# Kernel tuning notes

Hardware: AMD Instinct MI355X
Metric: run time of the kernel (lower is better)

## Reference

```python
import jax, jax.numpy as jnp
import numpy as np

# --- batched state-vector quantum circuit sim: AngleEmbedding(RY) + BasicEntanglerLayers(RX + ring CNOT) ---

def _ry(state, theta, wire, n):
    # per-sample RY(theta) on `wire`; state: (B,) + (2,)*n complex
    ax = wire + 1
    c = jnp.cos(0.5 * theta).reshape((-1,) + (1,) * (n - 1)).astype(state.dtype)
    s = jnp.sin(0.5 * theta).reshape((-1,) + (1,) * (n - 1)).astype(state.dtype)
    s0 = jnp.take(state, 0, axis=ax)
    s1 = jnp.take(state, 1, axis=ax)
    return jnp.stack([c * s0 - s * s1, s * s0 + c * s1], axis=ax)

def _rx(state, theta, wire, n):
    # scalar RX(theta) on `wire` (shared weight across batch)
    ax = wire + 1
    c = jnp.cos(0.5 * theta).astype(state.dtype)
    s = (-1j * jnp.sin(0.5 * theta)).astype(state.dtype)
    s0 = jnp.take(state, 0, axis=ax)
    s1 = jnp.take(state, 1, axis=ax)
    return jnp.stack([c * s0 + s * s1, s * s0 + c * s1], axis=ax)

def _cnot(state, ctrl, tgt):
    ax_c = ctrl + 1
    s0 = jnp.take(state, 0, axis=ax_c)
    s1 = jnp.take(state, 1, axis=ax_c)
    ax_t = tgt + 1 if tgt < ctrl else tgt  # target axis index after removing ctrl axis
    s1 = jnp.flip(s1, axis=ax_t)
    return jnp.stack([s0, s1], axis=ax_c)

def _circuit(x_qin, qweights):
    # x_qin: (Bn, n) angles; qweights: (L, n)
    Bn, n = x_qin.shape
    state = jnp.zeros((Bn,) + (2,) * n, jnp.complex64)
    state = state.at[(slice(None),) + (0,) * n].set(1.0)
    for w in range(n):  # AngleEmbedding, rotation='Y'
        state = _ry(state, x_qin[:, w], w, n)
    for l in range(qweights.shape[0]):  # BasicEntanglerLayers
        for w in range(n):
            state = _rx(state, qweights[l, w], w, n)
        for w in range(n):
            state = _cnot(state, w, (w + 1) % n)
    probs = jnp.real(state * jnp.conj(state))
    outs = []
    for w in range(n):  # <Z_w> = P(bit_w=0) - P(bit_w=1)
        axes = tuple(a for a in range(1, n + 1) if a != w + 1)
        p = probs.sum(axis=axes)  # (Bn, 2)
        outs.append(p[:, 0] - p[:, 1])
    return jnp.stack(outs, axis=-1).astype(jnp.float32)


def setup_inputs() -> dict:
    key = jax.random.key(0)
    ks = jax.random.split(key, 9)
    B, N, H, NQ, L = 16, 1024, 256, 8, 2
    x = jax.random.normal(ks[0], (B, N, H), jnp.float32)
    norm_adj = jax.random.uniform(ks[1], (N, N), jnp.float32) / N
    Wg = jax.random.normal(ks[2], (H, H), jnp.float32) * 0.02
    bg = jax.random.normal(ks[3], (H,), jnp.float32) * 0.02
    Wpre = jax.random.normal(ks[4], (NQ, H), jnp.float32) * 0.05
    bpre = jax.random.normal(ks[5], (NQ,), jnp.float32) * 0.02
    qweights = jax.random.uniform(ks[6], (L, NQ), jnp.float32) * (2.0 * np.pi)
    Wpost = jax.random.normal(ks[7], (H, NQ), jnp.float32) * 0.1
    bpost = jax.random.normal(ks[8], (H,), jnp.float32) * 0.02
    return {"x": x, "norm_adj": norm_adj, "Wg": Wg, "bg": bg, "Wpre": Wpre,
            "bpre": bpre, "qweights": qweights, "Wpost": Wpost, "bpost": bpost}


def reference(x, norm_adj, Wg, bg, Wpre, bpre, qweights, Wpost, bpost):
    # GCN aggregation + GELU(Linear)  (dropout is identity in eval mode)
    x_agg = jnp.einsum('ij,bjh->bih', norm_adj, x)
    x_agg = jax.nn.gelu(x_agg @ Wg.T + bg, approximate=False)
    B, N, H = x_agg.shape
    x_flat = x_agg.reshape(B * N, H).astype(jnp.float32)
    x_qin = jnp.tanh(x_flat @ Wpre.T + bpre) * np.pi
    q_out = _circuit(x_qin, qweights)          # (B*N, n_qubits)
    out = (q_out @ Wpost.T + bpost).reshape(B, N, H)
    return out
```

## Files before the change

### kernel.cpp

```cpp
#include <hip/hip_runtime.h>
#include <math.h>

typedef __attribute__((ext_vector_type(8))) short bf16x8;
typedef _Float16 f16x8 __attribute__((ext_vector_type(8)));
typedef __attribute__((ext_vector_type(4))) float f32x4;

#define PI_F 3.14159265358979323846f

__device__ __forceinline__ unsigned short f2bf(float f) {
  unsigned int u = __float_as_uint(f);
  u += 0x7FFFu + ((u >> 16) & 1u);
  return (unsigned short)(u >> 16);
}

__device__ __forceinline__ float bf2f(unsigned short u) {
  return __uint_as_float(((unsigned int)u) << 16);
}

__device__ __forceinline__ void async_ld16(const unsigned short* g, unsigned short* l) {
  __builtin_amdgcn_global_load_lds(
      (const __attribute__((address_space(1))) void*)g,
      (__attribute__((address_space(3))) void*)l,
      16, 0, 0);
}

__device__ __forceinline__ float fast_erf(float x) {
  float a = fabsf(x);
  float t = 1.0f / fmaf(0.3275911f, a, 1.0f);
  float p = t * fmaf(t, fmaf(t, fmaf(t, fmaf(t, 1.061405429f, -1.453152027f),
                                     1.421413741f), -0.284496736f), 0.254829592f);
  float e = __expf(-a * a);
  float r = 1.0f - p * e;
  return copysignf(r, x);
}

__device__ __forceinline__ float fast_tanh(float a) {
  float e = __expf(2.0f * a);
  return 1.0f - 2.0f / (e + 1.0f);
}

template<int ML, int MR>
__device__ __forceinline__ void apply_rx(float re[4], float im[4], float c, float s) {
  float pr[4], pi[4];
  #pragma unroll
  for (int r = 0; r < 4; r++) {
    float vr = re[r ^ MR], vi = im[r ^ MR];
    if (ML) { vr = __shfl_xor(vr, ML, 64); vi = __shfl_xor(vi, ML, 64); }
    pr[r] = vr; pi[r] = vi;
  }
  #pragma unroll
  for (int r = 0; r < 4; r++) {
    re[r] = fmaf(c, re[r],  s * pi[r]);
    im[r] = fmaf(c, im[r], -s * pr[r]);
  }
}

__global__ __launch_bounds__(256)
void prep_kernel(const float* __restrict__ adj, unsigned short* __restrict__ adj_bf,
                 const float* __restrict__ Wg, unsigned short* __restrict__ Wg_bf,
                 const float* __restrict__ qw, unsigned short* __restrict__ Uri,
                 const float* __restrict__ Wpost, _Float16* __restrict__ Gt,
                 const float* __restrict__ x, unsigned short* __restrict__ xT) {
  __shared__ float smem[1056];
  int bid = blockIdx.x, t = threadIdx.x;
  if (bid < 1024) {
    int i = bid * 256 + t;
    float4 v = ((const float4*)adj)[i];
    ushort4 o; o.x = f2bf(v.x); o.y = f2bf(v.y); o.z = f2bf(v.z); o.w = f2bf(v.w);
    ((ushort4*)adj_bf)[i] = o;
  } else if (bid < 1088) {
    int i = (bid - 1024) * 256 + t;
    float4 v = ((const float4*)Wg)[i];
    ushort4 o; o.x = f2bf(v.x); o.y = f2bf(v.y); o.z = f2bf(v.z); o.w = f2bf(v.w);
    ((ushort4*)Wg_bf)[i] = o;
  } else if (bid < 1152) {
    if (t < 16) { smem[t] = cosf(0.5f * qw[t]); smem[16 + t] = sinf(0.5f * qw[t]); }
    __syncthreads();
    int wv = t >> 6, L = t & 63;
    int k = (bid - 1088) * 4 + wv;
    float re[4], im[4];
    #pragma unroll
    for (int r = 0; r < 4; r++) { re[r] = (r * 64 + L == k) ? 1.f : 0.f; im[r] = 0.f; }
    apply_rx<1, 0>(re, im, smem[0], smem[16]);
    apply_rx<2, 0>(re, im, smem[1], smem[17]);
    apply_rx<4, 0>(re, im, smem[2], smem[18]);
    apply_rx<8, 0>(re, im, smem[3], smem[19]);
    apply_rx<16, 0>(re, im, smem[4], smem[20]);
    apply_rx<32, 0>(re, im, smem[5], smem[21]);
    apply_rx<0, 1>(re, im, smem[6], smem[22]);
    apply_rx<0, 2>(re, im, smem[7], smem[23]);
    apply_rx<3, 0>(re, im, smem[8], smem[24]);
    apply_rx<6, 0>(re, im, smem[9], smem[25]);
    apply_rx<12, 0>(re, im, smem[10], smem[26]);
    apply_rx<24, 0>(re, im, smem[11], smem[27]);
    apply_rx<48, 0>(re, im, smem[12], smem[28]);
    apply_rx<32, 1>(re, im, smem[13], smem[29]);
    apply_rx<0, 3>(re, im, smem[14], smem[30]);
    apply_rx<3, 2>(re, im, smem[15], smem[31]);
    const int M[8] = {0xAB, 0xFD, 0xFA, 0xF5, 0xEA, 0xD5, 0xAA, 0x55};
    #pragma unroll
    for (int r = 0; r < 4; r++) {
      int n = 0;
      #pragma unroll
      for (int w = 0; w < 8; w++) {
        int bit = (__popc(L & (M[w] & 63)) ^ __popc((r << 6) & M[w])) & 1;
        n |= bit << w;
      }
      int row_re = ((n >> 4) << 5) + (n & 15);
      Uri[(size_t)row_re * 256 + k] = f2bf(re[r]);
      Uri[(size_t)(row_re + 16) * 256 + k] = f2bf(im[r]);
    }
  } else if (bid < 1168) {
    int tid = (bid - 1152) * 256 + t;
    int h = tid >> 4;
    int n0 = (tid & 15) << 4;
    float wv8[8];
    #pragma unroll
    for (int w = 0; w < 8; w++) wv8[w] = Wpost[h * 8 + w];
    #pragma unroll
    for (int j = 0; j < 16; j++) {
      int n = n0 + j;
      float sum = 0.f;
      #pragma unroll
      for (int w = 0; w < 8; w++) sum += ((n >> w) & 1) ? -wv8[w] : wv8[w];
      Gt[h * 256 + n] = (_Float16)sum;
    }
  } else {
    int tb = bid - 1168;
    int jt = tb & 31, ht = (tb >> 5) & 7, bb = tb >> 8;
    int tx = t & 31, ty = t >> 5;
    const float* xb = x + (size_t)bb * 1024 * 256;
    #pragma unroll
    for (int i = 0; i < 4; i++) {
      int j = jt * 32 + ty + i * 8;
      smem[(ty + i * 8) * 33 + tx] = xb[(size_t)j * 256 + ht * 32 + tx];
    }
    __syncthreads();
    unsigned short* xTb = xT + (size_t)bb * 256 * 1024;
    #pragma unroll
    for (int i = 0; i < 4; i++) {
      int h = ht * 32 + ty + i * 8;
      xTb[(size_t)h * 1024 + jt * 32 + tx] = f2bf(smem[tx * 33 + ty + i * 8]);
    }
  }
}

__global__ __launch_bounds__(256)
void gemm1_kernel(const unsigned short* __restrict__ A,
                  const unsigned short* __restrict__ Bt,
                  unsigned short* __restrict__ C,
                  int K, int tilesN, int ldC) {
  __shared__ unsigned short As[2 * 64 * 32];
  __shared__ unsigned short Bs[2 * 128 * 32];
  int bid = blockIdx.x;
  int swz = (bid & 7) * 64 + (bid >> 3);
  int in_ = swz >> 4;
  int im  = swz & 15;
  const unsigned short* Ab  = A  + (long long)im * 64 * K;
  const unsigned short* Btb = Bt + (long long)in_ * 128 * K;

  int t = threadIdx.x;
  int wv = t >> 6, lane = t & 63;
  int wm = wv >> 1, wn = wv & 1;
  int l15 = lane & 15, quad = lane >> 4;

  f32x4 acc[2][4] = {};

  for (int kk = 0; kk < K; kk += 64) {
    __syncthreads();
    #pragma unroll
    for (int kb = 0; kb < 2; kb++) {
      {
        int r = t >> 2, c = (t & 3) ^ ((r >> 1) & 3);
        async_ld16(Ab + (long long)r * K + kk + kb * 32 + c * 8, &As[kb * 2048 + t * 8]);
      }
      #pragma unroll
      for (int q = 0; q < 2; q++) {
        int sidx = q * 256 + t;
        int r = sidx >> 2, c = (sidx & 3) ^ ((r >> 1) & 3);
        async_ld16(Btb + (long long)r * K + kk + kb * 32 + c * 8, &Bs[kb * 4096 + sidx * 8]);
      }
    }
    __syncthreads();
    #pragma unroll
    for (int kb = 0; kb < 2; kb++) {
      bf16x8 af[2], bfr[4];
      #pragma unroll
      for (int mt = 0; mt < 2; mt++) {
        int row = wm * 32 + mt * 16 + l15;
        af[mt] = *(const bf16x8*)&As[kb * 2048 + row * 32 + ((quad ^ ((row >> 1) & 3)) * 8)];
      }
      #pragma unroll
      for (int nt = 0; nt < 4; nt++) {
        int row = wn * 64 + nt * 16 + l15;
        bfr[nt] = *(const bf16x8*)&Bs[kb * 4096 + row * 32 + ((quad ^ ((row >> 1) & 3)) * 8)];
      }
      #pragma unroll
      for (int mt = 0; mt < 2; mt++)
        #pragma unroll
        for (int nt = 0; nt < 4; nt++)
          acc[mt][nt] = __builtin_amdgcn_mfma_f32_16x16x32_bf16(af[mt], bfr[nt], acc[mt][nt], 0, 0, 0);
    }
  }

  int n0 = in_ * 128;
  #pragma unroll
  for (int mt = 0; mt < 2; mt++) {
    #pragma unroll
    for (int nt = 0; nt < 4; nt++) {
      int colg = n0 + wn * 64 + nt * 16 + l15;
      #pragma unroll
      for (int r = 0; r < 4; r++) {
        int rowg = im * 64 + wm * 32 + mt * 16 + quad * 4 + r;
        C[(size_t)rowg * ldC + colg] = f2bf(acc[mt][nt][r]);
      }
    }
  }
}

__global__ __launch_bounds__(1024, 4)
void qfused_kernel(const unsigned short* __restrict__ xagg,
                   const unsigned short* __restrict__ Wg,
                   const float* __restrict__ bg,
                   const float* __restrict__ Wpre, const float* __restrict__ bpre,
                   const unsigned short* __restrict__ Uri,
                   const _Float16* __restrict__ Gt,
                   const float* __restrict__ bpost,
                   float* __restrict__ out) {
  __shared__ __align__(16) char smemraw[102400];
  unsigned short* As  = (unsigned short*)smemraw;
  unsigned short* gs  = (unsigned short*)(smemraw + 32768);
  _Float16*       Ts  = (_Float16*)(smemraw + 32768);
  unsigned short* P0s = (unsigned short*)(smemraw + 65536);
  float*          prt = (float*)(smemraw + 65536);
  float*          csw = (float*)(smemraw + 98304);

  int t = threadIdx.x;
  int wv = t >> 6, lane = t & 63;
  int l15 = lane & 15, quad = lane >> 4;

  const unsigned short* Ab = xagg + (size_t)blockIdx.x * 64 * 256;

  #pragma unroll
  for (int q = 0; q < 2; q++) {
    int sidx = q * 1024 + t;
    int kb = sidx >> 8;
    int r  = (sidx >> 2) & 63;
    int c  = (sidx & 3) ^ ((r >> 1) & 3);
    async_ld16(Ab + (size_t)r * 256 + kb * 32 + c * 8, &As[sidx * 8]);
  }
  __syncthreads();

  f32x4 acc[4] = {};
  {
    const unsigned short* Wp = Wg + (size_t)(wv * 16 + l15) * 256 + quad * 8;
    bf16x8 wf[2];
    wf[0] = *(const bf16x8*)(Wp);
    wf[1] = *(const bf16x8*)(Wp + 32);
    #pragma unroll
    for (int k8 = 0; k8 < 8; k8++) {
      int cur = k8 & 1;
      #pragma unroll
      for (int mt = 0; mt < 4; mt++) {
        int row = mt * 16 + l15;
        bf16x8 af = *(const bf16x8*)&As[k8 * 2048 + row * 32 + ((quad ^ ((row >> 1) & 3)) * 8)];
        acc[mt] = __builtin_amdgcn_mfma_f32_16x16x32_bf16(af, wf[cur], acc[mt], 0, 0, 0);
      }
      if (k8 < 6) wf[cur] = *(const bf16x8*)(Wp + (k8 + 2) * 32);
    }
  }
  {
    int col = wv * 16 + l15;
    float bgl = bg[col];
    int kbc = col >> 5, chunk = (col >> 3) & 3, e = col & 7;
    #pragma unroll
    for (int mt = 0; mt < 4; mt++) {
      #pragma unroll
      for (int r = 0; r < 4; r++) {
        int row = mt * 16 + quad * 4 + r;
        float v = acc[mt][r] + bgl;
        v = 0.5f * v * (1.0f + fast_erf(v * 0.7071067811865475f));
        *(unsigned short*)((char*)gs + kbc * 4096 + row * 64 +
                           ((chunk ^ ((row >> 1) & 3)) << 4) + e * 2) = f2bf(v);
      }
    }
  }
  __syncthreads();

  {
    int k8 = wv >> 1, mh = wv & 1;
    const float* wrow = Wpre + (size_t)(l15 & 7) * 256 + k8 * 32 + quad * 8;
    float4 wa = *(const float4*)wrow;
    float4 wb = *(const float4*)(wrow + 4);
    float v8[8] = {wa.x, wa.y, wa.z, wa.w, wb.x, wb.y, wb.z, wb.w};
    bf16x8 whi, wlo;
    #pragma unroll
    for (int j = 0; j < 8; j++) {
      unsigned short h = f2bf(v8[j]);
      whi[j] = (short)h;
      wlo[j] = (short)f2bf(v8[j] - bf2f(h));
    }
    f32x4 aacc[2] = {};
    #pragma unroll
    for (int mt = 0; mt < 2; mt++) {
      int row = mh * 32 + mt * 16 + l15;
      bf16x8 ga = *(const bf16x8*)((char*)gs + k8 * 4096 + row * 64 +
                                   ((quad ^ ((row >> 1) & 3)) << 4));
      aacc[mt] = __builtin_amdgcn_mfma_f32_16x16x32_bf16(ga, whi, aacc[mt], 0, 0, 0);
      aacc[mt] = __builtin_amdgcn_mfma_f32_16x16x32_bf16(ga, wlo, aacc[mt], 0, 0, 0);
    }
    if (l15 < 8) {
      #pragma unroll
      for (int mt = 0; mt < 2; mt++)
        #pragma unroll
        for (int r = 0; r < 4; r++)
          prt[k8 * 512 + (mh * 32 + mt * 16 + quad * 4 + r) * 8 + l15] = aacc[mt][r];
    }
  }
  __syncthreads();

  if (t < 512) {
    float s = 0.f;
    #pragma unroll
    for (int k = 0; k < 8; k++) s += prt[k * 512 + t];
    float th = (0.5f * PI_F) * fast_tanh(s + bpre[t & 7]);
    int row = t >> 3, w = t & 7;
    csw[row * 16 + w] = __cosf(th);
    csw[row * 16 + 8 + w] = __sinf(th);
  }
  __syncthreads();

  #pragma unroll
  for (int rr = 0; rr < 4; rr++) {
    int row = wv * 4 + rr;
    float4 c0 = *(const float4*)&csw[row * 16];
    float4 c1 = *(const float4*)&csw[row * 16 + 4];
    float4 s0 = *(const float4*)&csw[row * 16 + 8];
    float4 s1 = *(const float4*)&csw[row * 16 + 12];
    float cw[8] = {c0.x, c0.y, c0.z, c0.w, c1.x, c1.y, c1.z, c1.w};
    float sw[8] = {s0.x, s0.y, s0.z, s0.w, s1.x, s1.y, s1.z, s1.w};
    float pl = 1.f;
    #pragma unroll
    for (int b = 0; b < 6; b++) pl *= ((lane >> b) & 1) ? sw[b + 2] : cw[b + 2];
    ushort4 o;
    o.x = f2bf(pl * cw[0] * cw[1]);
    o.y = f2bf(pl * sw[0] * cw[1]);
    o.z = f2bf(pl * cw[0] * sw[1]);
    o.w = f2bf(pl * sw[0] * sw[1]);
    int jj = lane & 7;
    int cswz = (jj >> 1) ^ ((row >> 1) & 3);
    *(ushort4*)((char*)P0s + (lane >> 3) * 4096 + row * 64 + cswz * 16 + (jj & 1) * 8) = o;
  }
  __syncthreads();

  f32x4 acc1[4][2] = {};
  {
    const unsigned short* Up = Uri + (size_t)(wv * 32 + l15) * 256 + quad * 8;
    bf16x8 ua[2][2];
    #pragma unroll
    for (int sl = 0; sl < 2; sl++)
      #pragma unroll
      for (int nt = 0; nt < 2; nt++)
        ua[sl][nt] = *(const bf16x8*)(Up + sl * 32 + nt * 4096);
    #pragma unroll
    for (int k8 = 0; k8 < 8; k8++) {
      int cur = k8 & 1;
      #pragma unroll
      for (int mt = 0; mt < 4; mt++) {
        int row = mt * 16 + l15;
        bf16x8 pa = *(const bf16x8*)((char*)P0s + k8 * 4096 + row * 64 +
                                     ((quad ^ ((row >> 1) & 3)) << 4));
        acc1[mt][0] = __builtin_amdgcn_mfma_f32_16x16x32_bf16(pa, ua[cur][0], acc1[mt][0], 0, 0, 0);
        acc1[mt][1] = __builtin_amdgcn_mfma_f32_16x16x32_bf16(pa, ua[cur][1], acc1[mt][1], 0, 0, 0);
      }
      if (k8 < 6) {
        #pragma unroll
        for (int nt = 0; nt < 2; nt++)
          ua[cur][nt] = *(const bf16x8*)(Up + (k8 + 2) * 32 + nt * 4096);
      }
    }
  }

  {
    int colT = wv * 16 + l15;
    int kbc = colT >> 5, chunk = (colT >> 3) & 3, e = colT & 7;
    #pragma unroll
    for (int mt = 0; mt < 4; mt++) {
      #pragma unroll
      for (int r = 0; r < 4; r++) {
        int row = mt * 16 + quad * 4 + r;
        float tre = acc1[mt][0][r], tim = acc1[mt][1][r];
        *(_Float16*)((char*)Ts + kbc * 4096 + row * 64 +
                     ((chunk ^ ((row >> 1) & 3)) << 4) + e * 2)
            = (_Float16)(tre * tre + tim * tim);
      }
    }
  }
  __syncthreads();

  f32x4 acc2[4] = {};
  {
    const _Float16* Gp = Gt + (size_t)(wv * 16 + l15) * 256 + quad * 8;
    f16x8 gf[2];
    gf[0] = *(const f16x8*)(Gp);
    gf[1] = *(const f16x8*)(Gp + 32);
    #pragma unroll
    for (int k8 = 0; k8 < 8; k8++) {
      int cur = k8 & 1;
      #pragma unroll
      for (int mt = 0; mt < 4; mt++) {
        int row = mt * 16 + l15;
        f16x8 tf = *(const f16x8*)((char*)Ts + k8 * 4096 + row * 64 +
                                   ((quad ^ ((row >> 1) & 3)) << 4));
        acc2[mt] = __builtin_amdgcn_mfma_f32_16x16x32_f16(tf, gf[cur], acc2[mt], 0, 0, 0);
      }
      if (k8 < 6) gf[cur] = *(const f16x8*)(Gp + (k8 + 2) * 32);
    }
  }

  {
    int col = wv * 16 + l15;
    float bp = bpost[col];
    #pragma unroll
    for (int mt = 0; mt < 4; mt++) {
      #pragma unroll
      for (int r = 0; r < 4; r++) {
        int row = mt * 16 + quad * 4 + r;
        int s = blockIdx.x * 64 + row;
        int orow = (s & 15) * 1024 + (s >> 4);
        out[(size_t)orow * 256 + col] = acc2[mt][r] + bp;
      }
    }
  }
}

extern "C" void kernel_launch(void* const* d_in, const int* in_sizes, int n_in,
                              void* d_out, int out_size, void* d_ws, size_t ws_size,
                              hipStream_t stream) {
  const float* x     = (const float*)d_in[0];
  const float* adj   = (const float*)d_in[1];
  const float* Wg    = (const float*)d_in[2];
  const float* bg    = (const float*)d_in[3];
  const float* Wpre  = (const float*)d_in[4];
  const float* bpre  = (const float*)d_in[5];
  const float* qw    = (const float*)d_in[6];
  const float* Wpost = (const float*)d_in[7];
  const float* bpost = (const float*)d_in[8];
  float* out = (float*)d_out;

  char* ws = (char*)d_ws;
  unsigned short* adj_bf  = (unsigned short*)(ws + 0);
  unsigned short* Wg_bf   = (unsigned short*)(ws + 2097152);
  unsigned short* xT_bf   = (unsigned short*)(ws + 2228224);
  unsigned short* xagg_bf = (unsigned short*)(ws + 10616832);
  unsigned short* Uri     = (unsigned short*)(ws + 19005440);
  _Float16*       Gt      = (_Float16*)(ws + 19267584);

  prep_kernel<<<5264, 256, 0, stream>>>(adj, adj_bf, Wg, Wg_bf, qw, Uri,
                                        Wpost, Gt, x, xT_bf);

  gemm1_kernel<<<512, 256, 0, stream>>>(adj_bf, xT_bf, xagg_bf, 1024, 32, 4096);

  qfused_kernel<<<256, 1024, 0, stream>>>(xagg_bf, Wg_bf, bg, Wpre, bpre, Uri, Gt, bpost, out);
}
```

Before: 132.5 us.

## Double-buffer gemm1 LDS tiles and vectorize the x transpose loads/stores

The gemm1 kernel now uses two LDS buffers and issues the async global-to-LDS loads for the next K-step before computing on the current one. This is meant to overlap memory latency with MFMA work, and the per-step offset math is hoisted out of the loop. LDS use doubles, which can lower occupancy. Separately, the fp32-to-bf16 transpose in the prep kernel switches to float4 loads and ushort4 stores, so fewer, wider memory transactions are issued.

```diff
diff --git a/kernel.cpp b/kernel.cpp
--- a/kernel.cpp
+++ b/kernel.cpp
@@ -128,20 +128,24 @@
   } else {
     int tb = bid - 1168;
     int jt = tb & 31, ht = (tb >> 5) & 7, bb = tb >> 8;
-    int tx = t & 31, ty = t >> 5;
     const float* xb = x + (size_t)bb * 1024 * 256;
-    #pragma unroll
-    for (int i = 0; i < 4; i++) {
-      int j = jt * 32 + ty + i * 8;
-      smem[(ty + i * 8) * 33 + tx] = xb[(size_t)j * 256 + ht * 32 + tx];
+    int row = t >> 3, cg = t & 7;
+    {
+      float4 v = *(const float4*)&xb[(size_t)(jt * 32 + row) * 256 + ht * 32 + cg * 4];
+      smem[row * 33 + cg * 4 + 0] = v.x;
+      smem[row * 33 + cg * 4 + 1] = v.y;
+      smem[row * 33 + cg * 4 + 2] = v.z;
+      smem[row * 33 + cg * 4 + 3] = v.w;
     }
     __syncthreads();
     unsigned short* xTb = xT + (size_t)bb * 256 * 1024;
-    #pragma unroll
-    for (int i = 0; i < 4; i++) {
-      int h = ht * 32 + ty + i * 8;
-      xTb[(size_t)h * 1024 + jt * 32 + tx] = f2bf(smem[tx * 33 + ty + i * 8]);
-    }
+    int h = ht * 32 + row;
+    ushort4 o;
+    o.x = f2bf(smem[(cg * 4 + 0) * 33 + row]);
+    o.y = f2bf(smem[(cg * 4 + 1) * 33 + row]);
+    o.z = f2bf(smem[(cg * 4 + 2) * 33 + row]);
+    o.w = f2bf(smem[(cg * 4 + 3) * 33 + row]);
+    *(ushort4*)&xTb[(size_t)h * 1024 + jt * 32 + cg * 4] = o;
   }
 }
 
@@ -150,8 +154,8 @@
                   const unsigned short* __restrict__ Bt,
                   unsigned short* __restrict__ C,
                   int K, int tilesN, int ldC) {
-  __shared__ unsigned short As[2 * 64 * 32];
-  __shared__ unsigned short Bs[2 * 128 * 32];
+  __shared__ unsigned short As[2 * 2 * 64 * 32];
+  __shared__ unsigned short Bs[2 * 2 * 128 * 32];
   int bid = blockIdx.x;
   int swz = (bid & 7) * 64 + (bid >> 3);
   int in_ = swz >> 4;
@@ -164,36 +168,49 @@
   int wm = wv >> 1, wn = wv & 1;
   int l15 = lane & 15, quad = lane >> 4;
 
+  int ra  = t >> 2,        ca  = (t & 3) ^ ((ra >> 1) & 3);
+  int rb1 = (256 + t) >> 2, cb1 = ((256 + t) & 3) ^ ((rb1 >> 1) & 3);
+  long long goA  = (long long)ra * K + ca * 8;
+  long long goB0 = (long long)ra * K + ca * 8;
+  long long goB1 = (long long)rb1 * K + cb1 * 8;
+
   f32x4 acc[2][4] = {};
 
-  for (int kk = 0; kk < K; kk += 64) {
-    __syncthreads();
-    #pragma unroll
-    for (int kb = 0; kb < 2; kb++) {
-      {
-        int r = t >> 2, c = (t & 3) ^ ((r >> 1) & 3);
-        async_ld16(Ab + (long long)r * K + kk + kb * 32 + c * 8, &As[kb * 2048 + t * 8]);
-      }
-      #pragma unroll
-      for (int q = 0; q < 2; q++) {
-        int sidx = q * 256 + t;
-        int r = sidx >> 2, c = (sidx & 3) ^ ((r >> 1) & 3);
-        async_ld16(Btb + (long long)r * K + kk + kb * 32 + c * 8, &Bs[kb * 4096 + sidx * 8]);
-      }
-    }
-    __syncthreads();
+  #pragma unroll
+  for (int kb = 0; kb < 2; kb++) {
+    async_ld16(Ab + goA + kb * 32, &As[kb * 2048 + t * 8]);
+    async_ld16(Btb + goB0 + kb * 32, &Bs[kb * 4096 + t * 8]);
+    async_ld16(Btb + goB1 + kb * 32, &Bs[kb * 4096 + (256 + t) * 8]);
+  }
+  __syncthreads();
+
+  int nk = K >> 6;
+  for (int ki = 0; ki < nk; ki++) {
+    int buf = ki & 1;
+    if (ki + 1 < nk) {
+      int nb = buf ^ 1;
+      long long kk = (long long)(ki + 1) << 6;
+      #pragma unroll
+      for (int kb = 0; kb < 2; kb++) {
+        async_ld16(Ab + goA + kk + kb * 32, &As[nb * 4096 + kb * 2048 + t * 8]);
+        async_ld16(Btb + goB0 + kk + kb * 32, &Bs[nb * 8192 + kb * 4096 + t * 8]);
+        async_ld16(Btb + goB1 + kk + kb * 32, &Bs[nb * 8192 + kb * 4096 + (256 + t) * 8]);
+      }
+    }
     #pragma unroll
     for (int kb = 0; kb < 2; kb++) {
       bf16x8 af[2], bfr[4];
       #pragma unroll
       for (int mt = 0; mt < 2; mt++) {
         int row = wm * 32 + mt * 16 + l15;
-        af[mt] = *(const bf16x8*)&As[kb * 2048 + row * 32 + ((quad ^ ((row >> 1) & 3)) * 8)];
+        af[mt] = *(const bf16x8*)&As[buf * 4096 + kb * 2048 + row * 32 +
+                                     ((quad ^ ((row >> 1) & 3)) * 8)];
       }
       #pragma unroll
       for (int nt = 0; nt < 4; nt++) {
         int row = wn * 64 + nt * 16 + l15;
-        bfr[nt] = *(const bf16x8*)&Bs[kb * 4096 + row * 32 + ((quad ^ ((row >> 1) & 3)) * 8)];
+        bfr[nt] = *(const bf16x8*)&Bs[buf * 8192 + kb * 4096 + row * 32 +
+                                      ((quad ^ ((row >> 1) & 3)) * 8)];
       }
       #pragma unroll
       for (int mt = 0; mt < 2; mt++)
@@ -201,6 +218,7 @@
         for (int nt = 0; nt < 4; nt++)
           acc[mt][nt] = __builtin_amdgcn_mfma_f32_16x16x32_bf16(af[mt], bfr[nt], acc[mt][nt], 0, 0, 0);
     }
+    __syncthreads();
   }
 
   int n0 = in_ * 128;
```

After: 129.2 us. -2.5%, faster.
